# Kernel tuning notes

Hardware: AMD Instinct MI355X
Metric: run time of the kernel (lower is better)

## Reference

```python
import jax, jax.numpy as jnp
import numpy as np

B, L, H, VS = 128, 256, 128, 256  # vs = max(vocab_size, 2*H) = 256
THRESH = 0.4
EPS_NORM = 1e-12  # F.normalize eps
EPS_LN = 1e-5     # LayerNorm eps


def setup_inputs() -> dict:
    key = jax.random.key(0)
    ks = jax.random.split(key, 8)
    s = 0.02
    return {
        "seq": jax.random.randint(ks[0], (B, L), 0, VS),
        "embed": jax.random.normal(ks[1], (VS, H), dtype=jnp.float32) * s,
        "W1": jax.random.normal(ks[2], (2 * H, H), dtype=jnp.float32) * s,
        "b1": jnp.zeros((2 * H,), dtype=jnp.float32),
        "W2": jax.random.normal(ks[3], (H, 2 * H), dtype=jnp.float32) * s,
        "b2": jnp.zeros((H,), dtype=jnp.float32),
        "gamma": jnp.ones((H,), dtype=jnp.float32),
        "beta": jnp.zeros((H,), dtype=jnp.float32),
        "Wk": jax.random.normal(ks[4], (H, H), dtype=jnp.float32) * s,
        "Wr": jax.random.normal(ks[5], (H, H), dtype=jnp.float32) * s,
        "br": jnp.zeros((H,), dtype=jnp.float32),
        "Wo": jax.random.normal(ks[6], (VS, H), dtype=jnp.float32) * s,
        "bo": jnp.zeros((VS,), dtype=jnp.float32),
    }


def reference(seq, embed, W1, b1, W2, b2, gamma, beta, Wk, Wr, br, Wo, bo):
    # Embedding + FFN residual + LayerNorm
    h = embed[seq]                                    # (B,L,H)
    f = jax.nn.relu(h @ W1.T + b1) @ W2.T + b2        # (B,L,H)
    x = h + f
    mu = x.mean(-1, keepdims=True)
    var = x.var(-1, keepdims=True)                    # biased, matches torch LN
    h = (x - mu) / jnp.sqrt(var + EPS_LN) * gamma + beta

    # Precompute all keys, then sequential gated delta-rule update of M.
    K = h @ Wk.T                                      # (B,L,H), kp has no bias
    Kt = jnp.swapaxes(K, 0, 1)                        # (L,B,H)

    def step(M, k):                                   # M: (B,H,H), k: (B,H)
        kn = k / jnp.maximum(jnp.linalg.norm(k, axis=-1, keepdims=True), EPS_NORM)
        vp = jnp.einsum('bij,bj->bi', M, kn)          # predicted value
        err = k - vp
        d = err[:, :, None] * kn[:, None, :]          # outer-product write (B,H,H)
        # 'rel_norm' criterion: ||k - vp|| >= thresh * ||k||
        energy = jnp.linalg.norm(err, axis=-1)
        ref = THRESH * jnp.linalg.norm(k, axis=-1)
        g = (energy >= ref).astype(M.dtype)[:, None, None]
        return M + g * d, None

    M0 = jnp.zeros((B, H, H), dtype=h.dtype)
    M, _ = jax.lax.scan(step, M0, Kt[:-1])            # L-1 sequential steps

    q = Kt[-1]                                        # query from last position
    read = jnp.einsum('bij,bj->bi', M, q)             # (B,H)
    return (read @ Wr.T + br) @ Wo.T + bo             # (B,VS)
```

## Files before the change

kernel.cpp:

```cpp
#include <hip/hip_runtime.h>
#include <math.h>

#define B_   128
#define L_   256
#define H_   128
#define H2_  256
#define VS_  256

__device__ __forceinline__ float fma4(float4 a, float4 b, float acc) {
    acc = fmaf(a.x, b.x, acc);
    acc = fmaf(a.y, b.y, acc);
    acc = fmaf(a.z, b.z, acc);
    acc = fmaf(a.w, b.w, acc);
    return acc;
}

template <int CTRL>
__device__ __forceinline__ float dpp_add(float x) {
    int y = __builtin_amdgcn_update_dpp(0, __float_as_int(x), CTRL, 0xf, 0xf, true);
    return x + __int_as_float(y);
}
__device__ __forceinline__ float wave_sum(float x) {
    x = dpp_add<0x111>(x);
    x = dpp_add<0x112>(x);
    x = dpp_add<0x114>(x);
    x = dpp_add<0x118>(x);
    x = dpp_add<0x142>(x);
    x = dpp_add<0x143>(x);
    return x;
}
__device__ __forceinline__ float quad_sum(float x) {
    x = dpp_add<0xB1>(x);
    x = dpp_add<0x4E>(x);
    return x;
}

__global__ __launch_bounds__(256) void k_vffn(
    const float* __restrict__ embed,
    const float* __restrict__ W1, const float* __restrict__ b1,
    const float* __restrict__ W2, const float* __restrict__ b2,
    const float* __restrict__ gamma, const float* __restrict__ beta,
    const float* __restrict__ Wk, float* __restrict__ Fout)
{
    __shared__ float sh_h[4][128];
    __shared__ float sh_y[4][256];

    const int tid  = threadIdx.x;
    const int lane = tid & 63;
    const int r    = tid >> 6;
    const int v    = blockIdx.x * 4 + r;

    const float4* embed4 = (const float4*)embed;
    const float4* W1_4   = (const float4*)W1;
    const float4* W2_4   = (const float4*)W2;
    const float4* Wk_4   = (const float4*)Wk;

    if (lane < 32)
        *(float4*)&sh_h[r][lane * 4] = embed4[v * 32 + lane];
    __syncthreads();

    #pragma unroll
    for (int jj = 0; jj < 4; ++jj) {
        int j = jj * 64 + lane;
        const float4* wrow = W1_4 + j * 32;
        float acc = 0.f;
        #pragma unroll
        for (int c4 = 0; c4 < 32; ++c4)
            acc = fma4(*(const float4*)&sh_h[r][c4 * 4], wrow[c4], acc);
        sh_y[r][j] = fmaxf(acc + b1[j], 0.f);
    }
    __syncthreads();

    float xv[4];
    #pragma unroll
    for (int cc = 0; cc < 4; ++cc) {
        int c  = cc * 32 + (lane & 31);
        int hf = lane >> 5;
        const float4* wrow = W2_4 + c * 64 + hf * 32;
        float acc = 0.f;
        #pragma unroll
        for (int j4 = 0; j4 < 32; ++j4)
            acc = fma4(*(const float4*)&sh_y[r][(hf * 32 + j4) * 4], wrow[j4], acc);
        acc += __shfl_xor(acc, 32);
        xv[cc] = acc;
    }
    if (lane < 32) {
        #pragma unroll
        for (int cc = 0; cc < 4; ++cc) {
            int c = cc * 32 + lane;
            sh_h[r][c] = sh_h[r][c] + xv[cc] + b2[c];
        }
    }
    __syncthreads();

    {
        float2 x2 = *(const float2*)&sh_h[r][lane * 2];
        float s  = x2.x + x2.y;
        float s2 = x2.x * x2.x + x2.y * x2.y;
        s  += __shfl_xor(s, 1);  s  += __shfl_xor(s, 2);  s  += __shfl_xor(s, 4);
        s  += __shfl_xor(s, 8);  s  += __shfl_xor(s, 16); s  += __shfl_xor(s, 32);
        s2 += __shfl_xor(s2, 1); s2 += __shfl_xor(s2, 2); s2 += __shfl_xor(s2, 4);
        s2 += __shfl_xor(s2, 8); s2 += __shfl_xor(s2, 16); s2 += __shfl_xor(s2, 32);
        float mu   = s * (1.f / 128.f);
        float var  = s2 * (1.f / 128.f) - mu * mu;
        float rstd = 1.f / sqrtf(var + 1e-5f);
        float2 g2  = *(const float2*)&gamma[lane * 2];
        float2 be2 = *(const float2*)&beta[lane * 2];
        float2 o;
        o.x = (x2.x - mu) * rstd * g2.x + be2.x;
        o.y = (x2.y - mu) * rstd * g2.y + be2.y;
        *(float2*)&sh_h[r][lane * 2] = o;
    }
    __syncthreads();

    #pragma unroll
    for (int kk = 0; kk < 2; ++kk) {
        int k = kk * 64 + lane;
        const float4* wrow = Wk_4 + k * 32;
        float acc = 0.f;
        #pragma unroll
        for (int c4 = 0; c4 < 32; ++c4)
            acc = fma4(*(const float4*)&sh_h[r][c4 * 4], wrow[c4], acc);
        Fout[v * 128 + k] = acc;
    }
}

__global__ __launch_bounds__(512) void k_scan(
    const int* __restrict__ seq, const float* __restrict__ Fbuf,
    const float* __restrict__ Wr, const float* __restrict__ br,
    const float* __restrict__ Wo, const float* __restrict__ bo,
    float* __restrict__ out)
{
    extern __shared__ float smem_f[];
    float4* shk4  = (float4*)smem_f;
    float*  shkf  = smem_f;
    float*  rna   = smem_f + 32768;
    float*  thr   = rna + 256;
    float*  d01   = thr + 256;
    float*  red_f = d01 + 256;
    float*  rd_   = red_f + 16;
    float*  r2_   = rd_ + 128;

    const int tid  = threadIdx.x;
    const int lane = tid & 63;
    const int w    = tid >> 6;
    const int cq   = lane & 3;
    const int row  = w * 16 + (lane >> 2);
    const int b    = blockIdx.x;
    const float4* F4 = (const float4*)Fbuf;
    const int* seqb = seq + b * 256;

    for (int f = tid; f < 8192; f += 512) {
        int t = f >> 5, c = f & 31;
        shk4[f] = F4[(size_t)seqb[t] * 32 + c];
    }
    __syncthreads();

    {
        int rr = tid >> 4, cc = tid & 15;
        for (int it = 0; it < 8; ++it) {
            int t  = it * 32 + rr;
            int tn = (t < 255) ? t + 1 : 255;
            float4 a0 = shk4[t  * 32 + cc], a1 = shk4[t  * 32 + 16 + cc];
            float4 b0 = shk4[tn * 32 + cc], b1 = shk4[tn * 32 + 16 + cc];
            float n2p = fma4(a1, a1, fma4(a0, a0, 0.f));
            float cp  = fma4(a1, b1, fma4(a0, b0, 0.f));
            n2p += __shfl_xor(n2p, 1); n2p += __shfl_xor(n2p, 2);
            n2p += __shfl_xor(n2p, 4); n2p += __shfl_xor(n2p, 8);
            cp  += __shfl_xor(cp, 1);  cp  += __shfl_xor(cp, 2);
            cp  += __shfl_xor(cp, 4);  cp  += __shfl_xor(cp, 8);
            if (cc == 0) {
                rna[t] = 1.f / fmaxf(sqrtf(n2p), 1e-12f);
                thr[t] = 0.16f * n2p;
                d01[t] = cp;
            }
        }
    }

    float4 m[8];
    #pragma unroll
    for (int u = 0; u < 8; ++u) m[u] = make_float4(0.f, 0.f, 0.f, 0.f);

    float4 kbE[8], kbO[8];
    {
        const float4* ks0 = shk4 + cq * 8;
        const float4* ks1 = shk4 + 32 + cq * 8;
        #pragma unroll
        for (int u = 0; u < 8; ++u) {
            kbE[u] = ks0[(u + cq) & 7];
            kbO[u] = ks1[(u + cq) & 7];
        }
    }
    float errR = shkf[row];
    {
        float e2p = (cq == 0) ? errR * errR : 0.f;
        e2p = wave_sum(e2p);
        if (lane == 63) red_f[w] = e2p;
    }
    __syncthreads();

#define REGION(T, KU, KM)                                                       \
  {                                                                             \
    const int t_ = (T);                                                         \
    float rnaT = rna[t_], rnaN = rna[t_ + 1];                                   \
    float thrT = thr[t_], d01T = d01[t_];                                       \
    float kselfN = shkf[(t_ + 1) * 128 + row];                                  \
    float4 ra = ((const float4*)red_f)[(t_ & 1) * 2];                           \
    float4 rb = ((const float4*)red_f)[(t_ & 1) * 2 + 1];                       \
               \
    float pA = 0.f, pB = 0.f;                                                   \
    pA = fma4(m[0], KM[0], pA); pB = fma4(m[1], KM[1], pB);                     \
    pA = fma4(m[2], KM[2], pA); pB = fma4(m[3], KM[3], pB);                     \
    pA = fma4(m[4], KM[4], pA); pB = fma4(m[5], KM[5], pB);                     \
    pA = fma4(m[6], KM[6], pA); pB = fma4(m[7], KM[7], pB);                     \
    float preM = quad_sum(pA + pB);                                             \
    float E2 = ((ra.x + ra.y) + (ra.z + ra.w)) +                                \
               ((rb.x + rb.y) + (rb.z + rb.w));                                 \
    float a_ = (E2 >= thrT) ? rnaT * errR : 0.f;                                \
    float pre = fmaf(a_, d01T, preM);               \
    float errN = fmaf(-rnaN, pre, kselfN);                                      \
            \
    float e2p = errN * errN;                                                    \
    e2p = dpp_add<0x114>(e2p);                                  \
    e2p = dpp_add<0x118>(e2p);                                  \
    e2p = dpp_add<0x142>(e2p);                                \
    e2p = dpp_add<0x143>(e2p);                \
    if (lane == 63) red_f[((t_ + 1) & 1) * 8 + w] = e2p;                        \
    __builtin_amdgcn_sched_barrier(0);                                          \
        \
    _Pragma("unroll")                                                           \
    for (int u = 0; u < 8; ++u) {                                               \
      m[u].x = fmaf(a_, KU[u].x, m[u].x);                                       \
      m[u].y = fmaf(a_, KU[u].y, m[u].y);                                       \
      m[u].z = fmaf(a_, KU[u].z, m[u].z);                                       \
      m[u].w = fmaf(a_, KU[u].w, m[u].w);                                       \
    }                                                                           \
    {                                                                           \
      const float4* ks = shk4 + (t_ + 2) * 32 + cq * 8;                         \
      _Pragma("unroll")                                                         \
      for (int u = 0; u < 8; ++u) KU[u] = ks[(u + cq) & 7];                     \
    }                                                                           \
    __builtin_amdgcn_sched_barrier(0);                                          \
                        \
    asm volatile("s_waitcnt lgkmcnt(8)" ::: "memory");                          \
    __builtin_amdgcn_sched_barrier(0);                                          \
    __builtin_amdgcn_s_barrier();                                               \
    errR = errN;                                                                \
  }

    for (int tt = 0; tt < 254; tt += 2) {
        REGION(tt,     kbE, kbO);
        REGION(tt + 1, kbO, kbE);
    }
#undef REGION

    {
        float4 ra = ((const float4*)red_f)[0];
        float4 rb = ((const float4*)red_f)[1];
        float E2 = ((ra.x + ra.y) + (ra.z + ra.w)) +
                   ((rb.x + rb.y) + (rb.z + rb.w));
        float a_ = (E2 >= thr[254]) ? rna[254] * errR : 0.f;
        float pA = 0.f, pB = 0.f;
        pA = fma4(m[0], kbO[0], pA); pB = fma4(m[1], kbO[1], pB);
        pA = fma4(m[2], kbO[2], pA); pB = fma4(m[3], kbO[3], pB);
        pA = fma4(m[4], kbO[4], pA); pB = fma4(m[5], kbO[5], pB);
        pA = fma4(m[6], kbO[6], pA); pB = fma4(m[7], kbO[7], pB);
        float preM = quad_sum(pA + pB);
        float pre  = fmaf(a_, d01[254], preM);
        if (cq == 0) rd_[row] = pre;
    }
    __syncthreads();

    {
        int i = tid >> 2, q = tid & 3;
        const float4* Wr4 = (const float4*)Wr;
        const float4* rdv = (const float4*)rd_;
        float s = 0.f;
        #pragma unroll
        for (int u = 0; u < 8; ++u) s = fma4(rdv[q * 8 + u], Wr4[i * 32 + q * 8 + u], s);
        s += __shfl_xor(s, 1);
        s += __shfl_xor(s, 2);
        if (q == 0) r2_[i] = s + br[i];
    }
    __syncthreads();
    {
        int v = tid >> 1, h = tid & 1;
        const float4* Wo4 = (const float4*)Wo;
        const float4* r2v = (const float4*)r2_;
        float s = 0.f;
        #pragma unroll
        for (int u = 0; u < 16; ++u) s = fma4(r2v[h * 16 + u], Wo4[v * 32 + h * 16 + u], s);
        s += __shfl_xor(s, 1);
        if (h == 0) out[b * 256 + v] = s + bo[v];
    }
}

extern "C" void kernel_launch(void* const* d_in, const int* in_sizes, int n_in,
                              void* d_out, int out_size, void* d_ws, size_t ws_size,
                              hipStream_t stream) {
    const int*   seq   = (const int*)  d_in[0];
    const float* embed = (const float*)d_in[1];
    const float* W1    = (const float*)d_in[2];
    const float* b1    = (const float*)d_in[3];
    const float* W2    = (const float*)d_in[4];
    const float* b2    = (const float*)d_in[5];
    const float* gamma = (const float*)d_in[6];
    const float* beta  = (const float*)d_in[7];
    const float* Wk    = (const float*)d_in[8];
    const float* Wr    = (const float*)d_in[9];
    const float* br    = (const float*)d_in[10];
    const float* Wo    = (const float*)d_in[11];
    const float* bo    = (const float*)d_in[12];

    float* Fbuf = (float*)d_ws;
    float* out  = (float*)d_out;

    const size_t scan_lds = 32768 * 4 + 3 * 256 * 4 + 16 * 4 + 2 * 128 * 4;

    k_vffn<<<VS_ / 4, 256, 0, stream>>>(embed, W1, b1, W2, b2, gamma, beta, Wk, Fbuf);
    k_scan<<<B_, 512, scan_lds, stream>>>(seq, Fbuf, Wr, br, Wo, bo, out);
}
```

Baseline: 158.6 us.

## Re-tile scan state as 4 rows x 8 cols per lane with permuted key layout

The per-lane slice of the recurrent matrix M changes from 1 row x 32 columns (quad split) to 4 rows x 8 columns, with 16 lanes sharing a row group. Keys are stored in shared memory in a permuted column order so each lane loads only 2 float4 per step instead of 8, and each lane reads its own float4 of errors. The reductions become 16-lane DPP sums, and the rank-1 update is skipped when the gate is closed. This cuts LDS traffic and register pressure per step, but adds more cross-lane reduction work and a branch.

```diff
diff --git a/kernel.cpp b/kernel.cpp
--- a/kernel.cpp
+++ b/kernel.cpp
@@ -20,18 +20,11 @@
     int y = __builtin_amdgcn_update_dpp(0, __float_as_int(x), CTRL, 0xf, 0xf, true);
     return x + __int_as_float(y);
 }
-__device__ __forceinline__ float wave_sum(float x) {
-    x = dpp_add<0x111>(x);
-    x = dpp_add<0x112>(x);
-    x = dpp_add<0x114>(x);
-    x = dpp_add<0x118>(x);
-    x = dpp_add<0x142>(x);
-    x = dpp_add<0x143>(x);
-    return x;
-}
-__device__ __forceinline__ float quad_sum(float x) {
+__device__ __forceinline__ float group16_sum(float x) {
     x = dpp_add<0xB1>(x);
     x = dpp_add<0x4E>(x);
+    x = dpp_add<0x141>(x);
+    x = dpp_add<0x140>(x);
     return x;
 }
 
@@ -133,7 +126,6 @@
 {
     extern __shared__ float smem_f[];
     float4* shk4  = (float4*)smem_f;
-    float*  shkf  = smem_f;
     float*  rna   = smem_f + 32768;
     float*  thr   = rna + 256;
     float*  d01   = thr + 256;
@@ -144,15 +136,17 @@
     const int tid  = threadIdx.x;
     const int lane = tid & 63;
     const int w    = tid >> 6;
-    const int cq   = lane & 3;
-    const int row  = w * 16 + (lane >> 2);
+    const int cg   = lane & 15;
+    const int rg   = w * 4 + (lane >> 4);
     const int b    = blockIdx.x;
     const float4* F4 = (const float4*)Fbuf;
     const int* seqb = seq + b * 256;
+    const int kspos = ((rg & 1) * 16) | (rg >> 1);
 
     for (int f = tid; f < 8192; f += 512) {
-        int t = f >> 5, c = f & 31;
-        shk4[f] = F4[(size_t)seqb[t] * 32 + c];
+        int p = f & 31;
+        int c4 = ((p & 15) * 2) | (p >> 4);
+        shk4[f] = F4[(size_t)seqb[f >> 5] * 32 + c4];
     }
     __syncthreads();
 
@@ -177,25 +171,22 @@
         }
     }
 
-    float4 m[8];
+    float4 m[4][2];
     #pragma unroll
-    for (int u = 0; u < 8; ++u) m[u] = make_float4(0.f, 0.f, 0.f, 0.f);
-
-    float4 kbE[8], kbO[8];
-    {
-        const float4* ks0 = shk4 + cq * 8;
-        const float4* ks1 = shk4 + 32 + cq * 8;
-        #pragma unroll
-        for (int u = 0; u < 8; ++u) {
-            kbE[u] = ks0[(u + cq) & 7];
-            kbO[u] = ks1[(u + cq) & 7];
-        }
-    }
-    float errR = shkf[row];
-    {
-        float e2p = (cq == 0) ? errR * errR : 0.f;
-        e2p = wave_sum(e2p);
-        if (lane == 63) red_f[w] = e2p;
+    for (int r = 0; r < 4; ++r) {
+        m[r][0] = make_float4(0.f, 0.f, 0.f, 0.f);
+        m[r][1] = make_float4(0.f, 0.f, 0.f, 0.f);
+    }
+    float4 kbE[2], kbO[2];
+    kbE[0] = shk4[cg];        kbE[1] = shk4[16 + cg];
+    kbO[0] = shk4[32 + cg];   kbO[1] = shk4[32 + 16 + cg];
+    float4 errR = shk4[kspos];
+    {
+        float s = fmaf(errR.x, errR.x, fmaf(errR.y, errR.y,
+                  fmaf(errR.z, errR.z, errR.w * errR.w)));
+        s = dpp_add<0x142>(s);
+        s = dpp_add<0x143>(s);
+        if (lane == 63) red_f[w] = s;
     }
     __syncthreads();
 
@@ -204,45 +195,73 @@
     const int t_ = (T);                                                         \
     float rnaT = rna[t_], rnaN = rna[t_ + 1];                                   \
     float thrT = thr[t_], d01T = d01[t_];                                       \
-    float kselfN = shkf[(t_ + 1) * 128 + row];                                  \
+    float4 ksN = shk4[(t_ + 1) * 32 + kspos];       \
     float4 ra = ((const float4*)red_f)[(t_ & 1) * 2];                           \
     float4 rb = ((const float4*)red_f)[(t_ & 1) * 2 + 1];                       \
-               \
-    float pA = 0.f, pB = 0.f;                                                   \
-    pA = fma4(m[0], KM[0], pA); pB = fma4(m[1], KM[1], pB);                     \
-    pA = fma4(m[2], KM[2], pA); pB = fma4(m[3], KM[3], pB);                     \
-    pA = fma4(m[4], KM[4], pA); pB = fma4(m[5], KM[5], pB);                     \
-    pA = fma4(m[6], KM[6], pA); pB = fma4(m[7], KM[7], pB);                     \
-    float preM = quad_sum(pA + pB);                                             \
+             \
+    float p0 = fma4(m[0][1], KM[1], fma4(m[0][0], KM[0], 0.f));                 \
+    float p1 = fma4(m[1][1], KM[1], fma4(m[1][0], KM[0], 0.f));                 \
+    float p2 = fma4(m[2][1], KM[1], fma4(m[2][0], KM[0], 0.f));                 \
+    float p3 = fma4(m[3][1], KM[1], fma4(m[3][0], KM[0], 0.f));                 \
+    p0 = group16_sum(p0); p1 = group16_sum(p1);                                 \
+    p2 = group16_sum(p2); p3 = group16_sum(p3);                                 \
     float E2 = ((ra.x + ra.y) + (ra.z + ra.w)) +                                \
                ((rb.x + rb.y) + (rb.z + rb.w));                                 \
-    float a_ = (E2 >= thrT) ? rnaT * errR : 0.f;                                \
-    float pre = fmaf(a_, d01T, preM);               \
-    float errN = fmaf(-rnaN, pre, kselfN);                                      \
-            \
-    float e2p = errN * errN;                                                    \
-    e2p = dpp_add<0x114>(e2p);                                  \
-    e2p = dpp_add<0x118>(e2p);                                  \
-    e2p = dpp_add<0x142>(e2p);                                \
-    e2p = dpp_add<0x143>(e2p);                \
-    if (lane == 63) red_f[((t_ + 1) & 1) * 8 + w] = e2p;                        \
+    float gf = (E2 >= thrT) ? rnaT : 0.f;                                       \
+    float a0 = gf * errR.x, a1 = gf * errR.y;                                   \
+    float a2 = gf * errR.z, a3 = gf * errR.w;                                   \
+    float4 errN;                                                                \
+    errN.x = fmaf(-rnaN, fmaf(a0, d01T, p0), ksN.x);                            \
+    errN.y = fmaf(-rnaN, fmaf(a1, d01T, p1), ksN.y);                            \
+    errN.z = fmaf(-rnaN, fmaf(a2, d01T, p2), ksN.z);                            \
+    errN.w = fmaf(-rnaN, fmaf(a3, d01T, p3), ksN.w);                            \
+    float s = fmaf(errN.x, errN.x, fmaf(errN.y, errN.y,                         \
+              fmaf(errN.z, errN.z, errN.w * errN.w)));                          \
+    s = dpp_add<0x142>(s);                                                      \
+    s = dpp_add<0x143>(s);                                                      \
+    if (lane == 63) red_f[((t_ + 1) & 1) * 8 + w] = s;                          \
     __builtin_amdgcn_sched_barrier(0);                                          \
-        \
-    _Pragma("unroll")                                                           \
-    for (int u = 0; u < 8; ++u) {                                               \
-      m[u].x = fmaf(a_, KU[u].x, m[u].x);                                       \
-      m[u].y = fmaf(a_, KU[u].y, m[u].y);                                       \
-      m[u].z = fmaf(a_, KU[u].z, m[u].z);                                       \
-      m[u].w = fmaf(a_, KU[u].w, m[u].w);                                       \
+             \
+    if (gf != 0.f) {                                                            \
+      m[0][0].x = fmaf(a0, KU[0].x, m[0][0].x);                                 \
+      m[0][0].y = fmaf(a0, KU[0].y, m[0][0].y);                                 \
+      m[0][0].z = fmaf(a0, KU[0].z, m[0][0].z);                                 \
+      m[0][0].w = fmaf(a0, KU[0].w, m[0][0].w);                                 \
+      m[0][1].x = fmaf(a0, KU[1].x, m[0][1].x);                                 \
+      m[0][1].y = fmaf(a0, KU[1].y, m[0][1].y);                                 \
+      m[0][1].z = fmaf(a0, KU[1].z, m[0][1].z);                                 \
+      m[0][1].w = fmaf(a0, KU[1].w, m[0][1].w);                                 \
+      m[1][0].x = fmaf(a1, KU[0].x, m[1][0].x);                                 \
+      m[1][0].y = fmaf(a1, KU[0].y, m[1][0].y);                                 \
+      m[1][0].z = fmaf(a1, KU[0].z, m[1][0].z);                                 \
+      m[1][0].w = fmaf(a1, KU[0].w, m[1][0].w);                                 \
+      m[1][1].x = fmaf(a1, KU[1].x, m[1][1].x);                                 \
+      m[1][1].y = fmaf(a1, KU[1].y, m[1][1].y);                                 \
+      m[1][1].z = fmaf(a1, KU[1].z, m[1][1].z);                                 \
+      m[1][1].w = fmaf(a1, KU[1].w, m[1][1].w);                                 \
+      m[2][0].x = fmaf(a2, KU[0].x, m[2][0].x);                                 \
+      m[2][0].y = fmaf(a2, KU[0].y, m[2][0].y);                                 \
+      m[2][0].z = fmaf(a2, KU[0].z, m[2][0].z);                                 \
+      m[2][0].w = fmaf(a2, KU[0].w, m[2][0].w);                                 \
+      m[2][1].x = fmaf(a2, KU[1].x, m[2][1].x);                                 \
+      m[2][1].y = fmaf(a2, KU[1].y, m[2][1].y);                                 \
+      m[2][1].z = fmaf(a2, KU[1].z, m[2][1].z);                                 \
+      m[2][1].w = fmaf(a2, KU[1].w, m[2][1].w);                                 \
+      m[3][0].x = fmaf(a3, KU[0].x, m[3][0].x);                                 \
+      m[3][0].y = fmaf(a3, KU[0].y, m[3][0].y);                                 \
+      m[3][0].z = fmaf(a3, KU[0].z, m[3][0].z);                                 \
+      m[3][0].w = fmaf(a3, KU[0].w, m[3][0].w);                                 \
+      m[3][1].x = fmaf(a3, KU[1].x, m[3][1].x);                                 \
+      m[3][1].y = fmaf(a3, KU[1].y, m[3][1].y);                                 \
+      m[3][1].z = fmaf(a3, KU[1].z, m[3][1].z);                                 \
+      m[3][1].w = fmaf(a3, KU[1].w, m[3][1].w);                                 \
     }                                                                           \
-    {                                                                           \
-      const float4* ks = shk4 + (t_ + 2) * 32 + cq * 8;                         \
-      _Pragma("unroll")                                                         \
-      for (int u = 0; u < 8; ++u) KU[u] = ks[(u + cq) & 7];                     \
-    }                                                                           \
+                                                \
+    KU[0] = shk4[(t_ + 2) * 32 + cg];                                           \
+    KU[1] = shk4[(t_ + 2) * 32 + 16 + cg];                                      \
     __builtin_amdgcn_sched_barrier(0);                                          \
-                        \
-    asm volatile("s_waitcnt lgkmcnt(8)" ::: "memory");                          \
+                            \
+    asm volatile("s_waitcnt lgkmcnt(2)" ::: "memory");                          \
     __builtin_amdgcn_sched_barrier(0);                                          \
     __builtin_amdgcn_s_barrier();                                               \
     errR = errN;                                                                \
@@ -259,15 +278,20 @@
         float4 rb = ((const float4*)red_f)[1];
         float E2 = ((ra.x + ra.y) + (ra.z + ra.w)) +
                    ((rb.x + rb.y) + (rb.z + rb.w));
-        float a_ = (E2 >= thr[254]) ? rna[254] * errR : 0.f;
-        float pA = 0.f, pB = 0.f;
-        pA = fma4(m[0], kbO[0], pA); pB = fma4(m[1], kbO[1], pB);
-        pA = fma4(m[2], kbO[2], pA); pB = fma4(m[3], kbO[3], pB);
-        pA = fma4(m[4], kbO[4], pA); pB = fma4(m[5], kbO[5], pB);
-        pA = fma4(m[6], kbO[6], pA); pB = fma4(m[7], kbO[7], pB);
-        float preM = quad_sum(pA + pB);
-        float pre  = fmaf(a_, d01[254], preM);
-        if (cq == 0) rd_[row] = pre;
+        float gf = (E2 >= thr[254]) ? rna[254] : 0.f;
+        float d01T = d01[254];
+        float p0 = fma4(m[0][1], kbO[1], fma4(m[0][0], kbO[0], 0.f));
+        float p1 = fma4(m[1][1], kbO[1], fma4(m[1][0], kbO[0], 0.f));
+        float p2 = fma4(m[2][1], kbO[1], fma4(m[2][0], kbO[0], 0.f));
+        float p3 = fma4(m[3][1], kbO[1], fma4(m[3][0], kbO[0], 0.f));
+        p0 = group16_sum(p0); p1 = group16_sum(p1);
+        p2 = group16_sum(p2); p3 = group16_sum(p3);
+        float4 pre;
+        pre.x = fmaf(gf * errR.x, d01T, p0);
+        pre.y = fmaf(gf * errR.y, d01T, p1);
+        pre.z = fmaf(gf * errR.z, d01T, p2);
+        pre.w = fmaf(gf * errR.w, d01T, p3);
+        if (cg == 0) *(float4*)&rd_[rg * 4] = pre;
     }
     __syncthreads();
 
```

After: 166.7 us. +5.1%, slower.

## Stream keys from global Fbuf via token indices instead of staging in LDS

Applied to the files above, without the earlier changes.

Drops the 128 KB LDS staging of the gathered per-token key rows. The scan now reads keys straight from the global (L2-resident) Fbuf table through a small shared copy of the sequence indices, prefetching the next key vector and the scalar self-key a few steps ahead with a rotating 3-register buffer. The goal is to remove the upfront gather and the large LDS footprint, but it puts global-memory latency onto the serial critical path of each scan step. The LDS wait is also tightened to lgkmcnt(0) and the matrix update is reordered before the reduction.

```diff
diff --git a/kernel.cpp b/kernel.cpp
--- a/kernel.cpp
+++ b/kernel.cpp
@@ -131,15 +131,13 @@
     const float* __restrict__ Wo, const float* __restrict__ bo,
     float* __restrict__ out)
 {
-    extern __shared__ float smem_f[];
-    float4* shk4  = (float4*)smem_f;
-    float*  shkf  = smem_f;
-    float*  rna   = smem_f + 32768;
-    float*  thr   = rna + 256;
-    float*  d01   = thr + 256;
-    float*  red_f = d01 + 256;
-    float*  rd_   = red_f + 16;
-    float*  r2_   = rd_ + 128;
+    __shared__ float rna[256];
+    __shared__ float thr[256];
+    __shared__ float d01[256];
+    __shared__ float red_f[16];
+    __shared__ float rd_[128];
+    __shared__ float r2_[128];
+    __shared__ int   seqb_[256];
 
     const int tid  = threadIdx.x;
     const int lane = tid & 63;
@@ -148,12 +146,8 @@
     const int row  = w * 16 + (lane >> 2);
     const int b    = blockIdx.x;
     const float4* F4 = (const float4*)Fbuf;
-    const int* seqb = seq + b * 256;
-
-    for (int f = tid; f < 8192; f += 512) {
-        int t = f >> 5, c = f & 31;
-        shk4[f] = F4[(size_t)seqb[t] * 32 + c];
-    }
+
+    if (tid < 256) seqb_[tid] = seq[b * 256 + tid];
     __syncthreads();
 
     {
@@ -161,8 +155,10 @@
         for (int it = 0; it < 8; ++it) {
             int t  = it * 32 + rr;
             int tn = (t < 255) ? t + 1 : 255;
-            float4 a0 = shk4[t  * 32 + cc], a1 = shk4[t  * 32 + 16 + cc];
-            float4 b0 = shk4[tn * 32 + cc], b1 = shk4[tn * 32 + 16 + cc];
+            const float4* A  = F4 + (size_t)seqb_[t]  * 32;
+            const float4* Bp = F4 + (size_t)seqb_[tn] * 32;
+            float4 a0 = A[cc],  a1 = A[16 + cc];
+            float4 b0 = Bp[cc], b1 = Bp[16 + cc];
             float n2p = fma4(a1, a1, fma4(a0, a0, 0.f));
             float cp  = fma4(a1, b1, fma4(a0, b0, 0.f));
             n2p += __shfl_xor(n2p, 1); n2p += __shfl_xor(n2p, 2);
@@ -183,15 +179,15 @@
 
     float4 kbE[8], kbO[8];
     {
-        const float4* ks0 = shk4 + cq * 8;
-        const float4* ks1 = shk4 + 32 + cq * 8;
-        #pragma unroll
-        for (int u = 0; u < 8; ++u) {
-            kbE[u] = ks0[(u + cq) & 7];
-            kbO[u] = ks1[(u + cq) & 7];
-        }
-    }
-    float errR = shkf[row];
+        const float4* p0 = F4 + (size_t)seqb_[0] * 32 + cq * 8;
+        const float4* p1 = F4 + (size_t)seqb_[1] * 32 + cq * 8;
+        #pragma unroll
+        for (int u = 0; u < 8; ++u) { kbE[u] = p0[u]; kbO[u] = p1[u]; }
+    }
+    float errR = Fbuf[(size_t)seqb_[0] * 128 + row];
+    float ksA  = Fbuf[(size_t)seqb_[1] * 128 + row];
+    float ksB  = Fbuf[(size_t)seqb_[2] * 128 + row];
+    float ksC  = Fbuf[(size_t)seqb_[3] * 128 + row];
     {
         float e2p = (cq == 0) ? errR * errR : 0.f;
         e2p = wave_sum(e2p);
@@ -199,12 +195,11 @@
     }
     __syncthreads();
 
-#define REGION(T, KU, KM)                                                       \
+#define REGION(T, KU, KM, KS)                                                   \
   {                                                                             \
     const int t_ = (T);                                                         \
     float rnaT = rna[t_], rnaN = rna[t_ + 1];                                   \
     float thrT = thr[t_], d01T = d01[t_];                                       \
-    float kselfN = shkf[(t_ + 1) * 128 + row];                                  \
     float4 ra = ((const float4*)red_f)[(t_ & 1) * 2];                           \
     float4 rb = ((const float4*)red_f)[(t_ & 1) * 2 + 1];                       \
                \
@@ -218,8 +213,23 @@
                ((rb.x + rb.y) + (rb.z + rb.w));                                 \
     float a_ = (E2 >= thrT) ? rnaT * errR : 0.f;                                \
     float pre = fmaf(a_, d01T, preM);               \
-    float errN = fmaf(-rnaN, pre, kselfN);                                      \
-            \
+    float errN = fmaf(-rnaN, pre, KS);                                          \
+                                             \
+    _Pragma("unroll")                                                           \
+    for (int u = 0; u < 8; ++u) {                                               \
+      m[u].x = fmaf(a_, KU[u].x, m[u].x);                                       \
+      m[u].y = fmaf(a_, KU[u].y, m[u].y);                                       \
+      m[u].z = fmaf(a_, KU[u].z, m[u].z);                                       \
+      m[u].w = fmaf(a_, KU[u].w, m[u].w);                                       \
+    }                                                                           \
+                 \
+    {                                                                           \
+      const float4* ks = F4 + (size_t)seqb_[t_ + 2] * 32 + cq * 8;              \
+      _Pragma("unroll")                                                         \
+      for (int u = 0; u < 8; ++u) KU[u] = ks[u];                                \
+    }                                                                           \
+    KS = Fbuf[(size_t)seqb_[(t_ + 4 > 255) ? 255 : t_ + 4] * 128 + row];        \
+                      \
     float e2p = errN * errN;                                                    \
     e2p = dpp_add<0x114>(e2p);                                  \
     e2p = dpp_add<0x118>(e2p);                                  \
@@ -227,31 +237,23 @@
     e2p = dpp_add<0x143>(e2p);                \
     if (lane == 63) red_f[((t_ + 1) & 1) * 8 + w] = e2p;                        \
     __builtin_amdgcn_sched_barrier(0);                                          \
-        \
-    _Pragma("unroll")                                                           \
-    for (int u = 0; u < 8; ++u) {                                               \
-      m[u].x = fmaf(a_, KU[u].x, m[u].x);                                       \
-      m[u].y = fmaf(a_, KU[u].y, m[u].y);                                       \
-      m[u].z = fmaf(a_, KU[u].z, m[u].z);                                       \
-      m[u].w = fmaf(a_, KU[u].w, m[u].w);                                       \
-    }                                                                           \
-    {                                                                           \
-      const float4* ks = shk4 + (t_ + 2) * 32 + cq * 8;                         \
-      _Pragma("unroll")                                                         \
-      for (int u = 0; u < 8; ++u) KU[u] = ks[(u + cq) & 7];                     \
-    }                                                                           \
-    __builtin_amdgcn_sched_barrier(0);                                          \
-                        \
-    asm volatile("s_waitcnt lgkmcnt(8)" ::: "memory");                          \
+    asm volatile("s_waitcnt lgkmcnt(0)" ::: "memory");                          \
     __builtin_amdgcn_sched_barrier(0);                                          \
     __builtin_amdgcn_s_barrier();                                               \
+    __builtin_amdgcn_sched_barrier(0);                                          \
     errR = errN;                                                                \
   }
 
-    for (int tt = 0; tt < 254; tt += 2) {
-        REGION(tt,     kbE, kbO);
-        REGION(tt + 1, kbO, kbE);
-    }
+    for (int tt = 0; tt < 252; tt += 6) {
+        REGION(tt + 0, kbE, kbO, ksA);
+        REGION(tt + 1, kbO, kbE, ksB);
+        REGION(tt + 2, kbE, kbO, ksC);
+        REGION(tt + 3, kbO, kbE, ksA);
+        REGION(tt + 4, kbE, kbO, ksB);
+        REGION(tt + 5, kbO, kbE, ksC);
+    }
+    REGION(252, kbE, kbO, ksA);
+    REGION(253, kbO, kbE, ksB);
 #undef REGION
 
     {
@@ -315,8 +317,6 @@
     float* Fbuf = (float*)d_ws;
     float* out  = (float*)d_out;
 
-    const size_t scan_lds = 32768 * 4 + 3 * 256 * 4 + 16 * 4 + 2 * 128 * 4;
-
     k_vffn<<<VS_ / 4, 256, 0, stream>>>(embed, W1, b1, W2, b2, gamma, beta, Wk, Fbuf);
-    k_scan<<<B_, 512, scan_lds, stream>>>(seq, Fbuf, Wr, br, Wo, bo, out);
-}
+    k_scan<<<B_, 512, 0, stream>>>(seq, Fbuf, Wr, br, Wo, bo, out);
+}
```

New measurement: 499.1 us. 3.15x slower.
